# Kernel tuning notes

Hardware: AMD Instinct MI355X
Metric: run time of the kernel (lower is better)

Reference implementation:

```python
import jax, jax.numpy as jnp
import numpy as np

B, C, OUT, H, W, M1, M2, HID = 4, 64, 64, 256, 256, 32, 32, 64
COORD = C + 1  # MLP input: channels + 1 coordinate


def _lin(key, fan_in, fan_out):
    lim = 1.0 / np.sqrt(fan_in)
    kw, kb = jax.random.split(key)
    Wm = jax.random.uniform(kw, (fan_in, fan_out), minval=-lim, maxval=lim, dtype=jnp.float32)
    b = jax.random.uniform(kb, (fan_out,), minval=-lim, maxval=lim, dtype=jnp.float32)
    return Wm, b


def setup_inputs() -> dict:
    key = jax.random.key(0)
    ks = jax.random.split(key, 12)
    x = jax.random.normal(ks[0], (B, C, H, W), dtype=jnp.float32)
    # basis_w MLP: (C+1) -> HID -> HID -> 2*M2
    wW0, wb0 = _lin(ks[1], COORD, HID)
    wW1, wb1 = _lin(ks[2], HID, HID)
    wW2, wb2 = _lin(ks[3], HID, 2 * M2)
    # basis_h MLP: (C+1) -> HID -> HID -> 2*M1
    hW0, hb0 = _lin(ks[4], COORD, HID)
    hW1, hb1 = _lin(ks[5], HID, HID)
    hW2, hb2 = _lin(ks[6], HID, 2 * M1)
    std = (1.0 / (C + OUT)) ** 0.5
    Wf_re = std * jax.random.normal(ks[7], (C, OUT, M1, M2), dtype=jnp.float32)
    Wf_im = std * jax.random.normal(ks[8], (C, OUT, M1, M2), dtype=jnp.float32)
    mixer_w, mixer_b = _lin(ks[9], OUT, OUT)
    mixer_w = mixer_w.T  # (out, in) conv1x1 layout
    sc_w, sc_b = _lin(ks[10], C, OUT)
    sc_w = sc_w.T
    return {
        "x": x,
        "wW0": wW0, "wb0": wb0, "wW1": wW1, "wb1": wb1, "wW2": wW2, "wb2": wb2,
        "hW0": hW0, "hb0": hb0, "hW1": hW1, "hb1": hb1, "hW2": hW2, "hb2": hb2,
        "Wf_re": Wf_re, "Wf_im": Wf_im,
        "mixer_w": mixer_w, "mixer_b": mixer_b,
        "sc_w": sc_w, "sc_b": sc_b,
    }


def _gelu(v):
    return jax.nn.gelu(v, approximate=False)  # torch GELU is exact erf


def _cmlp(x, W0, b0, W1, b1, W2, b2, m):
    h = _gelu(x @ W0 + b0)
    h = _gelu(h @ W1 + b1)
    o = h @ W2 + b2
    return jax.lax.complex(o[..., :m], o[..., m:])


def reference(x, wW0, wb0, wW1, wb1, wW2, wb2,
              hW0, hb0, hW1, hb1, hW2, hb2,
              Wf_re, Wf_im, mixer_w, mixer_b, sc_w, sc_b):
    Bb, Cc, Hh, Ww = x.shape
    # --- W-direction basis: input is (values, w-coord) per pixel ---
    wc = jnp.linspace(-1.0, 1.0, Ww, dtype=jnp.float32)
    w_in = jnp.concatenate(
        [jnp.transpose(x, (0, 2, 3, 1)),
         jnp.broadcast_to(wc[None, None, :, None], (Bb, Hh, Ww, 1))], axis=-1)
    wb = _cmlp(w_in, wW0, wb0, wW1, wb1, wW2, wb2, M2)  # (B,H,W,m2) complex
    xc = x.astype(jnp.complex64)
    # separable transform along W: contract W against runtime basis
    tfw = jnp.einsum('bchw,bhwm->bchm', xc, wb)  # (B,C,H,m2)
    # --- H-direction basis: input is real part of W-transform + h-coord ---
    hcv = jnp.linspace(-1.0, 1.0, Hh, dtype=jnp.float32)
    h_in = jnp.concatenate(
        [jnp.transpose(tfw.real, (0, 3, 2, 1)),
         jnp.broadcast_to(hcv[None, None, :, None], (Bb, M2, Hh, 1))], axis=-1)
    hb = _cmlp(h_in, hW0, hb0, hW1, hb1, hW2, hb2, M1)  # (B,m2,H,m1) complex
    tfhw = jnp.einsum('bchm,bmhk->bckm', tfw, hb)  # (B,C,m1,m2)
    Wf = jax.lax.complex(Wf_re, Wf_im)  # (C_in, C_out, m1, m2)
    proc = jnp.einsum('bixy,oixy->boxy', tfhw, Wf)  # (B,out,m1,m2)
    # inverse transforms with conjugate-transposed bases
    rec = jnp.einsum('bokm,bmhk->bohm', proc, jnp.conj(hb))  # (B,out,H,m2)
    spatial = jnp.einsum('bohm,bhwm->bohw', rec, jnp.conj(wb)).real / (Hh * Ww)
    y = jnp.einsum('bchw,oc->bohw', spatial, mixer_w) + mixer_b[None, :, None, None]
    y = _gelu(y)
    y = y + jnp.einsum('bchw,oc->bohw', x, sc_w) + sc_b[None, :, None, None]
    return _gelu(y)
```

## Files before the change

kernel.cpp:

```cpp
#include <hip/hip_runtime.h>
#include <math.h>


typedef __attribute__((ext_vector_type(8))) short bf16x8;
typedef __attribute__((ext_vector_type(4))) float f32x4;

__device__ __forceinline__ float gelu_f(float v) {
    const float u = v * 0.70710678118654752440f;
    const float xa = fabsf(u);
    const float t = __builtin_amdgcn_rcpf(fmaf(0.3275911f, xa, 1.0f));
    float p = fmaf(1.061405429f, t, -1.453152027f);
    p = fmaf(p, t, 1.421413741f);
    p = fmaf(p, t, -0.284496736f);
    p = fmaf(p, t, 0.254829592f);
    p *= t;
    const float e = __expf(-xa * xa);
    float erfv = fmaf(-p, e, 1.0f);
    erfv = (u < 0.0f) ? -erfv : erfv;
    return 0.5f * v * (1.0f + erfv);
}

__device__ __forceinline__ unsigned short f2b(float f) {
    union { float f; unsigned int u; } v; v.f = f;
    unsigned int u = v.u + 0x7FFFu + ((v.u >> 16) & 1u);
    return (unsigned short)(u >> 16);
}
__device__ __forceinline__ float b2f(unsigned short b) {
    union { unsigned int u; float f; } v; v.u = ((unsigned int)b) << 16;
    return v.f;
}

__device__ __forceinline__ ushort4 butterfly_xT(const float4 v, int q) {
    const float bx = __shfl_xor(v.x, 1);
    const float by = __shfl_xor(v.y, 1);
    const float bz = __shfl_xor(v.z, 1);
    const float bw = __shfl_xor(v.w, 1);
    float4 s1;
    s1.x = ((q & 1) == 0) ? v.x : by;
    s1.y = ((q & 1) == 0) ? bx  : v.y;
    s1.z = ((q & 1) == 0) ? v.z : bw;
    s1.w = ((q & 1) == 0) ? bz  : v.w;
    const float cx = __shfl_xor(s1.x, 2);
    const float cy = __shfl_xor(s1.y, 2);
    const float cz = __shfl_xor(s1.z, 2);
    const float cw = __shfl_xor(s1.w, 2);
    float4 s2;
    s2.x = ((q & 2) == 0) ? s1.x : cz;
    s2.y = ((q & 2) == 0) ? s1.y : cw;
    s2.z = ((q & 2) == 0) ? cx   : s1.z;
    s2.w = ((q & 2) == 0) ? cy   : s1.w;
    ushort4 u;
    u.x = f2b(s2.x); u.y = f2b(s2.y); u.z = f2b(s2.z); u.w = f2b(s2.w);
    return u;
}

__device__ __forceinline__ void stage_xT(const float* __restrict__ x,
    unsigned short* __restrict__ sA, int b, int h, int w0, int t, int LD)
{
    const int lane = t & 63, wv = t >> 6;
    const int q = lane & 3, wg = lane >> 2;
#pragma unroll
    for (int r = 0; r < 4; ++r) {
        const int cb = (r * 4 + wv) * 4;
        const float4 v = *(const float4*)&x[((size_t)(b * 64 + cb + q) * 256 + h) * 256 + w0 + wg * 4];
        const ushort4 u = butterfly_xT(v, q);
        *(ushort4*)&sA[(wg * 4 + q) * LD + cb] = u;
    }
}

__global__ void k_prep(const float* __restrict__ wW0, const float* __restrict__ wW1,
                       const float* __restrict__ wW2,
                       const float* __restrict__ hW0, const float* __restrict__ hW1,
                       const float* __restrict__ hW2,
                       unsigned short* __restrict__ wT0, unsigned short* __restrict__ wT1,
                       unsigned short* __restrict__ wT2,
                       unsigned short* __restrict__ hT0, unsigned short* __restrict__ hT1,
                       unsigned short* __restrict__ hT2)
{
    const int t = threadIdx.x;
    for (int idx = t; idx < 64 * 96; idx += 256) {
        const int o = idx / 96, k = idx % 96;
        wT0[idx] = (k < 65) ? f2b(wW0[k * 64 + o]) : (unsigned short)0;
        hT0[idx] = (k < 65) ? f2b(hW0[k * 64 + o]) : (unsigned short)0;
    }
    for (int idx = t; idx < 4096; idx += 256) {
        const int o = idx >> 6, k = idx & 63;
        wT1[idx] = f2b(wW1[k * 64 + o]);
        wT2[idx] = f2b(wW2[k * 64 + o]);
        hT1[idx] = f2b(hW1[k * 64 + o]);
        hT2[idx] = f2b(hW2[k * 64 + o]);
    }
}

__global__ __launch_bounds__(256) void k_psum(const float* __restrict__ src,
                                              float* __restrict__ dst,
                                              int nparts, int part_stride)
{
    const int i = (blockIdx.x * 256 + threadIdx.x) * 4;
    float4 acc = *(const float4*)&src[i];
    for (int p = 1; p < nparts; ++p) {
        const float4 v = *(const float4*)&src[(size_t)p * part_stride + i];
        acc.x += v.x; acc.y += v.y; acc.z += v.z; acc.w += v.w;
    }
    *(float4*)&dst[i] = acc;
}

__global__ __launch_bounds__(256) void k_psum_procT(const float* __restrict__ src,
                                                    float* __restrict__ dst)
{
    const int idx = blockIdx.x * 256 + threadIdx.x;
    const int o = idx & 63, k = (idx >> 6) & 31, m = (idx >> 11) & 31, b = idx >> 16;
    const size_t in = (size_t)(b * 64 + o) * 1024 + k * 32 + m;
    const float re = src[in] + src[524288 + in];
    const float im = src[262144 + in] + src[524288 + 262144 + in];
    dst[idx] = re;
    dst[262144 + idx] = im;
}

template<bool GELU, int NKC>
__device__ __forceinline__ void mfma_layer_r(
    const bf16x8* __restrict__ wf,
    const unsigned short* __restrict__ sAct,
    unsigned short* __restrict__ dst,
    const float4 bv, int arow, int g, int wv)
{
    const int crow = 16 * wv + g * 4;
    const int sx7 = arow & 7, sx3 = arow & 3;
    const f32x4 zero = {0.f, 0.f, 0.f, 0.f};
    f32x4 acc[4] = {zero, zero, zero, zero};
#pragma unroll
    for (int kc = 0; kc < NKC; ++kc) {
        const int chraw = kc * 4 + g;
        const int ch = (chraw < 8) ? (chraw ^ sx7) : (8 + ((chraw - 8) ^ sx3));
#pragma unroll
        for (int nt = 0; nt < 4; ++nt) {
            const bf16x8 b = *(const bf16x8*)&sAct[(nt * 16 + arow) * 96 + ch * 8];
            acc[nt] = __builtin_amdgcn_mfma_f32_16x16x32_bf16(wf[kc], b, acc[nt], 0, 0, 0);
        }
    }
    const int chw = (crow >> 3) ^ sx7;
#pragma unroll
    for (int nt = 0; nt < 4; ++nt) {
        const int px = nt * 16 + arow;
        float v0 = acc[nt][0] + bv.x;
        float v1 = acc[nt][1] + bv.y;
        float v2 = acc[nt][2] + bv.z;
        float v3 = acc[nt][3] + bv.w;
        if (GELU) { v0 = gelu_f(v0); v1 = gelu_f(v1); v2 = gelu_f(v2); v3 = gelu_f(v3); }
        ushort4 u;
        u.x = f2b(v0); u.y = f2b(v1); u.z = f2b(v2); u.w = f2b(v3);
        *(ushort4*)&dst[px * 96 + chw * 8 + (crow & 7)] = u;
    }
}

__device__ __forceinline__ float4 load_xtile(const float* __restrict__ x,
    int b, int h, int w0, int lane, int wv, int r)
{
    const int q = lane & 3, wg = lane >> 2;
    const int cb = 16 * r + 4 * wv;
    return *(const float4*)&x[((size_t)(b * 64 + cb + q) * 256 + h) * 256 + w0 + wg * 4];
}

__global__ __launch_bounds__(256) void k_wbtfw(
    const float* __restrict__ x,
    const unsigned short* __restrict__ wT0, const float* __restrict__ b0,
    const unsigned short* __restrict__ wT1, const float* __restrict__ b1,
    const unsigned short* __restrict__ wT2, const float* __restrict__ b2,
    unsigned short* __restrict__ wb_bf, unsigned short* __restrict__ tfwM)
{
    __shared__ __align__(16) unsigned short smem[20480];
    unsigned short* sA   = smem;
    unsigned short* sB   = smem + 6144;
    unsigned short* sXt  = smem + 12288;
    unsigned short* sWBt = smem + 16384;

    const int bh = blockIdx.x;
    const int b = bh >> 8, h = bh & 255;
    const int t = threadIdx.x;
    const int lane = t & 63, wv = t >> 6;
    const int arow = lane & 15, g = lane >> 4;
    const int crow = 16 * wv + g * 4;
    const int sx7 = arow & 7;
    const f32x4 zero = {0.f, 0.f, 0.f, 0.f};

    const int wrow = 16 * wv + arow;
    bf16x8 w0f[3], w1f[2], w2f[2];
#pragma unroll
    for (int kc = 0; kc < 3; ++kc)
        w0f[kc] = *(const bf16x8*)&wT0[wrow * 96 + (kc * 4 + g) * 8];
#pragma unroll
    for (int kc = 0; kc < 2; ++kc) {
        w1f[kc] = *(const bf16x8*)&wT1[wrow * 64 + (kc * 4 + g) * 8];
        w2f[kc] = *(const bf16x8*)&wT2[wrow * 64 + (kc * 4 + g) * 8];
    }
    const float4 bv0 = *(const float4*)&b0[crow];
    const float4 bv1 = *(const float4*)&b1[crow];
    const float4 bv2 = *(const float4*)&b2[crow];

    f32x4 atf[4] = {zero, zero, zero, zero};

    float4 xv[4];
#pragma unroll
    for (int r = 0; r < 4; ++r) xv[r] = load_xtile(x, b, h, 0, lane, wv, r);

    for (int wq = 0; wq < 4; ++wq) {
        const int w0 = wq * 64;
        __syncthreads();
        {
            const int q = lane & 3, wg = lane >> 2;
#pragma unroll
            for (int r = 0; r < 4; ++r) {
                const int cb = 16 * r + 4 * wv;
                const int c = cb + q;
                const float4 v = xv[r];
                ushort4 ux;
                ux.x = f2b(v.x); ux.y = f2b(v.y); ux.z = f2b(v.z); ux.w = f2b(v.w);
                const int chx = (wg >> 1) ^ (c & 7);
                *(ushort4*)&sXt[c * 64 + chx * 8 + 4 * (wg & 1)] = ux;
                const ushort4 u = butterfly_xT(v, q);
                const int row = wg * 4 + q;
                const int cha = (cb >> 3) ^ (row & 7);
                *(ushort4*)&sA[row * 96 + cha * 8 + (cb & 7)] = u;
            }
        }
        if (t < 64) {
            const uint4 z = {0, 0, 0, 0};
#pragma unroll
            for (int j = 0; j < 4; ++j)
                *(uint4*)&sA[t * 96 + (8 + (j ^ (t & 3))) * 8] = z;
            sA[t * 96 + (8 + (t & 3)) * 8] = f2b((float)(w0 + t) * (2.0f / 255.0f) - 1.0f);
        }
        const int w0n = ((wq + 1) & 3) * 64;
        float4 xn[4];
#pragma unroll
        for (int r = 0; r < 4; ++r) xn[r] = load_xtile(x, b, h, w0n, lane, wv, r);
        __syncthreads();
        mfma_layer_r<true, 3>(w0f, sA, sB, bv0, arow, g, wv);
        __syncthreads();
        mfma_layer_r<true, 2>(w1f, sB, sA, bv1, arow, g, wv);
        __syncthreads();
        {
            f32x4 acc[4] = {zero, zero, zero, zero};
#pragma unroll
            for (int kc = 0; kc < 2; ++kc) {
                const int ch = (kc * 4 + g) ^ sx7;
#pragma unroll
                for (int nt = 0; nt < 4; ++nt) {
                    const bf16x8 bb = *(const bf16x8*)&sA[(nt * 16 + arow) * 96 + ch * 8];
                    acc[nt] = __builtin_amdgcn_mfma_f32_16x16x32_bf16(w2f[kc], bb, acc[nt], 0, 0, 0);
                }
            }
            const int chw = (crow >> 3) ^ sx7;
#pragma unroll
            for (int nt = 0; nt < 4; ++nt) {
                const int px = nt * 16 + arow;
                ushort4 u;
                u.x = f2b(acc[nt][0] + bv2.x);
                u.y = f2b(acc[nt][1] + bv2.y);
                u.z = f2b(acc[nt][2] + bv2.z);
                u.w = f2b(acc[nt][3] + bv2.w);
                *(ushort4*)&sB[px * 96 + chw * 8 + (crow & 7)] = u;
                const int ph = px >> 3, pl = px & 7;
                sWBt[(crow + 0) * 64 + ((ph ^ ((crow + 0) & 7)) << 3) + pl] = u.x;
                sWBt[(crow + 1) * 64 + ((ph ^ ((crow + 1) & 7)) << 3) + pl] = u.y;
                sWBt[(crow + 2) * 64 + ((ph ^ ((crow + 2) & 7)) << 3) + pl] = u.z;
                sWBt[(crow + 3) * 64 + ((ph ^ ((crow + 3) & 7)) << 3) + pl] = u.w;
            }
        }
        __syncthreads();
        const size_t pixbase = (size_t)(b * 256 + h) * 256 + w0;
#pragma unroll
        for (int r = 0; r < 2; ++r) {
            const int idx = r * 256 + t;
            const int px = idx >> 3, f = idx & 7;
            *(uint4*)&wb_bf[(pixbase + px) * 64 + f * 8] =
                *(const uint4*)&sB[px * 96 + ((f ^ (px & 7)) << 3)];
        }
#pragma unroll
        for (int kc = 0; kc < 2; ++kc) {
            const int ch = (kc * 4 + g) ^ sx7;
            const bf16x8 a = *(const bf16x8*)&sWBt[(16 * wv + arow) * 64 + ch * 8];
#pragma unroll
            for (int nt = 0; nt < 4; ++nt) {
                const bf16x8 bb = *(const bf16x8*)&sXt[(nt * 16 + arow) * 64 + ch * 8];
                atf[nt] = __builtin_amdgcn_mfma_f32_16x16x32_bf16(a, bb, atf[nt], 0, 0, 0);
            }
        }
#pragma unroll
        for (int r = 0; r < 4; ++r) xv[r] = xn[r];
    }

    __syncthreads();
    float* sF = (float*)smem;
#pragma unroll
    for (int nt = 0; nt < 4; ++nt) {
        const int c = nt * 16 + arow;
#pragma unroll
        for (int j = 0; j < 4; ++j)
            sF[(crow + j) * 68 + c] = atf[nt][j];
    }
    __syncthreads();
#pragma unroll
    for (int r = 0; r < 4; ++r) {
        const int idx = r * 256 + t;
        const int m = idx >> 5, gg = idx & 31;
        ushort4 u;
        u.x = f2b(sF[m * 68 + gg * 2]);
        u.y = f2b(sF[(m + 32) * 68 + gg * 2]);
        u.z = f2b(sF[m * 68 + gg * 2 + 1]);
        u.w = f2b(sF[(m + 32) * 68 + gg * 2 + 1]);
        *(ushort4*)&tfwM[((size_t)(b * 32 + m) * 256 + h) * 128 + gg * 4] = u;
    }
}

__global__ __launch_bounds__(256) void k_hb_mlp3(
    const unsigned short* __restrict__ tfwM,
    const unsigned short* __restrict__ hT0, const float* __restrict__ b0,
    const unsigned short* __restrict__ hT1, const float* __restrict__ b1,
    const unsigned short* __restrict__ hT2, const float* __restrict__ b2,
    unsigned short* __restrict__ hb_bf)
{
    __shared__ __align__(16) unsigned short sA[64 * 96];
    __shared__ __align__(16) unsigned short sB[64 * 96];
    const int blk = blockIdx.x;
    const int bm = blk >> 2, hq = blk & 3;
    const int h0 = hq * 64;
    const int t = threadIdx.x;
    const int lane = t & 63, wv = t >> 6;
    const int arow = lane & 15, g = lane >> 4;
    const int crow = 16 * wv + g * 4;

    const int wrow = 16 * wv + arow;
    bf16x8 h0f[3], h1f[2], h2f[2];
#pragma unroll
    for (int kc = 0; kc < 3; ++kc)
        h0f[kc] = *(const bf16x8*)&hT0[wrow * 96 + (kc * 4 + g) * 8];
#pragma unroll
    for (int kc = 0; kc < 2; ++kc) {
        h1f[kc] = *(const bf16x8*)&hT1[wrow * 64 + (kc * 4 + g) * 8];
        h2f[kc] = *(const bf16x8*)&hT2[wrow * 64 + (kc * 4 + g) * 8];
    }
    const float4 bv0 = *(const float4*)&b0[crow];
    const float4 bv1 = *(const float4*)&b1[crow];
    const float4 bv2 = *(const float4*)&b2[crow];

#pragma unroll
    for (int r = 0; r < 4; ++r) {
        const int idx = r * 256 + t;
        const int p = idx >> 4, f = idx & 15;
        const uint4 raw = *(const uint4*)&tfwM[((size_t)(bm * 256 + h0 + p)) * 128 + f * 8];
        const unsigned short* s = (const unsigned short*)&raw;
        ushort4 u;
        u.x = s[0]; u.y = s[2]; u.z = s[4]; u.w = s[6];
        const int ch = (f >> 1) ^ (p & 7);
        *(ushort4*)&sA[p * 96 + ch * 8 + 4 * (f & 1)] = u;
    }
    if (t < 64) {
        const uint4 z = {0, 0, 0, 0};
#pragma unroll
        for (int j = 0; j < 4; ++j)
            *(uint4*)&sA[t * 96 + (8 + (j ^ (t & 3))) * 8] = z;
        sA[t * 96 + (8 + (t & 3)) * 8] = f2b((float)(h0 + t) * (2.0f / 255.0f) - 1.0f);
    }
    __syncthreads();
    mfma_layer_r<true, 3>(h0f, sA, sB, bv0, arow, g, wv);
    __syncthreads();
    mfma_layer_r<true, 2>(h1f, sB, sA, bv1, arow, g, wv);
    __syncthreads();
    mfma_layer_r<false, 2>(h2f, sA, sB, bv2, arow, g, wv);
    __syncthreads();

    const size_t pixbase = (size_t)bm * 256 + h0;
#pragma unroll
    for (int r = 0; r < 2; ++r) {
        const int idx = r * 256 + t;
        const int px = idx >> 3, f = idx & 7;
        *(uint4*)&hb_bf[(pixbase + px) * 64 + f * 8] =
            *(const uint4*)&sB[px * 96 + ((f ^ (px & 7)) << 3)];
    }
}

__global__ __launch_bounds__(256) void k_tfhw3(
    const unsigned short* __restrict__ tfwM,
    const unsigned short* __restrict__ hb_bf,
    float* __restrict__ tfhw_p)
{
    __shared__ float hr[64 * 32];
    __shared__ float hi2[64 * 32];
    __shared__ float slab[32 * 64];
    const int blk = blockIdx.x;
    const int bm = blk >> 3, chalf = (blk >> 2) & 1, hq = blk & 3;
    const int b = bm >> 5, m = bm & 31;
    const int t = threadIdx.x;
#pragma unroll
    for (int r = 0; r < 2; ++r) {
        const int q = r * 256 + t;
        const int hl = q >> 3, f = q & 7;
        const uint4 raw = *(const uint4*)&hb_bf[((size_t)bm * 256 + hq * 64 + hl) * 64 + f * 8];
        const unsigned short* us = (const unsigned short*)&raw;
        float v[8];
#pragma unroll
        for (int j = 0; j < 8; ++j) v[j] = b2f(us[j]);
        float* dst = (f < 4) ? &hr[hl * 32 + f * 8] : &hi2[hl * 32 + (f - 4) * 8];
        float4 lo; lo.x = v[0]; lo.y = v[1]; lo.z = v[2]; lo.w = v[3];
        float4 hi; hi.x = v[4]; hi.y = v[5]; hi.z = v[6]; hi.w = v[7];
        *(float4*)&dst[0] = lo;
        *(float4*)&dst[4] = hi;
    }
    const int k = t & 31, cq = t >> 5;
    float accr[4] = {0.f, 0.f, 0.f, 0.f}, acci[4] = {0.f, 0.f, 0.f, 0.f};
    const size_t tbase = (size_t)bm * 32768;
    for (int ht = 0; ht < 2; ++ht) {
        __syncthreads();
        {
            const int hl = t >> 3, f = t & 7;
            const uint4 raw = *(const uint4*)&tfwM[tbase + (size_t)(hq * 64 + ht * 32 + hl) * 128 + chalf * 64 + f * 8];
            const unsigned short* s = (const unsigned short*)&raw;
            float4 lo, hi;
            lo.x = b2f(s[0]); lo.y = b2f(s[1]); lo.z = b2f(s[2]); lo.w = b2f(s[3]);
            hi.x = b2f(s[4]); hi.y = b2f(s[5]); hi.z = b2f(s[6]); hi.w = b2f(s[7]);
            *(float4*)&slab[hl * 64 + f * 8] = lo;
            *(float4*)&slab[hl * 64 + f * 8 + 4] = hi;
        }
        __syncthreads();
#pragma unroll 8
        for (int hl = 0; hl < 32; ++hl) {
            const float hrv = hr[(ht * 32 + hl) * 32 + k];
            const float hiv = hi2[(ht * 32 + hl) * 32 + k];
            const float4 u0 = *(const float4*)&slab[hl * 64 + cq * 8];
            const float4 u1 = *(const float4*)&slab[hl * 64 + cq * 8 + 4];
            accr[0] = fmaf(u0.x, hrv, fmaf(-u0.y, hiv, accr[0]));
            acci[0] = fmaf(u0.x, hiv, fmaf( u0.y, hrv, acci[0]));
            accr[1] = fmaf(u0.z, hrv, fmaf(-u0.w, hiv, accr[1]));
            acci[1] = fmaf(u0.z, hiv, fmaf( u0.w, hrv, acci[1]));
            accr[2] = fmaf(u1.x, hrv, fmaf(-u1.y, hiv, accr[2]));
            acci[2] = fmaf(u1.x, hiv, fmaf( u1.y, hrv, acci[2]));
            accr[3] = fmaf(u1.z, hrv, fmaf(-u1.w, hiv, accr[3]));
            acci[3] = fmaf(u1.z, hiv, fmaf( u1.w, hrv, acci[3]));
        }
    }
    float* tp = tfhw_p + (size_t)hq * 524288;
#pragma unroll
    for (int i = 0; i < 4; ++i) {
        const int c = chalf * 32 + cq * 4 + i;
        const size_t po = ((size_t)(b * 64 + c) * 32 + k) * 32 + m;
        tp[po] = accr[i];
        tp[262144 + po] = acci[i];
    }
}

__global__ __launch_bounds__(256) void k_proc2(
    const float* __restrict__ tfhw,
    const float* __restrict__ Wf_re, const float* __restrict__ Wf_im,
    float* __restrict__ proc_p)
{
    const int blk = blockIdx.x;
    const int o = blk >> 3, kq = (blk >> 1) & 3, chalf = blk & 1;
    const int t = threadIdx.x;
    const int mo = kq * 256 + t;
    const float* tre = tfhw;
    const float* tim = tfhw + 262144;
    float accr[4] = {0.f, 0.f, 0.f, 0.f}, acci[4] = {0.f, 0.f, 0.f, 0.f};
    for (int cc = 0; cc < 32; ++cc) {
        const int c = chalf * 32 + cc;
        const float wfr = Wf_re[(size_t)(c * 64 + o) * 1024 + mo];
        const float wfi = Wf_im[(size_t)(c * 64 + o) * 1024 + mo];
#pragma unroll
        for (int bb = 0; bb < 4; ++bb) {
            const float tr = tre[(size_t)(bb * 64 + c) * 1024 + mo];
            const float ti = tim[(size_t)(bb * 64 + c) * 1024 + mo];
            accr[bb] = fmaf(tr, wfr, fmaf(-ti, wfi, accr[bb]));
            acci[bb] = fmaf(tr, wfi, fmaf(ti, wfr, acci[bb]));
        }
    }
    float* pp = proc_p + (size_t)chalf * 524288;
#pragma unroll
    for (int bb = 0; bb < 4; ++bb) {
        pp[(size_t)(bb * 64 + o) * 1024 + mo] = accr[bb];
        pp[262144 + (size_t)(bb * 64 + o) * 1024 + mo] = acci[bb];
    }
}

__global__ __launch_bounds__(256) void k_rec4(
    const float* __restrict__ procT,
    const unsigned short* __restrict__ hb_bf,
    unsigned short* __restrict__ recO)
{
    __shared__ float lhr[32 * 32];
    __shared__ float lhi[32 * 32];
    const int blk = blockIdx.x;
    const int bm = blk >> 3, hq = blk & 7;
    const int b = bm >> 5, m = bm & 31;
    const int t = threadIdx.x;
    {
        const int hl = t >> 3, f = t & 7;
        const uint4 raw = *(const uint4*)&hb_bf[((size_t)bm * 256 + hq * 32 + hl) * 64 + f * 8];
        const unsigned short* us = (const unsigned short*)&raw;
        float v[8];
#pragma unroll
        for (int j = 0; j < 8; ++j) v[j] = b2f(us[j]);
        float* dst = (f < 4) ? &lhr[hl * 32 + f * 8] : &lhi[hl * 32 + (f - 4) * 8];
        float4 lo; lo.x = v[0]; lo.y = v[1]; lo.z = v[2]; lo.w = v[3];
        float4 hi; hi.x = v[4]; hi.y = v[5]; hi.z = v[6]; hi.w = v[7];
        *(float4*)&dst[0] = lo;
        *(float4*)&dst[4] = hi;
    }
    const int o = t & 63, hg = t >> 6;
    const float* pr = procT + (size_t)(b * 32 + m) * 2048 + o;
    const float* pi = pr + 262144;
    float Pr[32], Pi[32];
#pragma unroll
    for (int k = 0; k < 32; ++k) {
        Pr[k] = pr[k * 64];
        Pi[k] = pi[k * 64];
    }
    __syncthreads();
    for (int hh = 0; hh < 8; ++hh) {
        const int hl = hg * 8 + hh;
        float ar = 0.f, ai = 0.f;
#pragma unroll
        for (int k4 = 0; k4 < 8; ++k4) {
            const float4 hr4 = *(const float4*)&lhr[hl * 32 + k4 * 4];
            const float4 hi4 = *(const float4*)&lhi[hl * 32 + k4 * 4];
            ar = fmaf(Pr[k4*4+0], hr4.x, fmaf(Pi[k4*4+0], hi4.x, ar));
            ai = fmaf(Pi[k4*4+0], hr4.x, fmaf(-Pr[k4*4+0], hi4.x, ai));
            ar = fmaf(Pr[k4*4+1], hr4.y, fmaf(Pi[k4*4+1], hi4.y, ar));
            ai = fmaf(Pi[k4*4+1], hr4.y, fmaf(-Pr[k4*4+1], hi4.y, ai));
            ar = fmaf(Pr[k4*4+2], hr4.z, fmaf(Pi[k4*4+2], hi4.z, ar));
            ai = fmaf(Pi[k4*4+2], hr4.z, fmaf(-Pr[k4*4+2], hi4.z, ai));
            ar = fmaf(Pr[k4*4+3], hr4.w, fmaf(Pi[k4*4+3], hi4.w, ar));
            ai = fmaf(Pi[k4*4+3], hr4.w, fmaf(-Pr[k4*4+3], hi4.w, ai));
        }
        const int h = hq * 32 + hl;
        const size_t rb = ((size_t)(b * 256 + h) * 64 + o) * 64;
        recO[rb + m]      = f2b(ar);
        recO[rb + 32 + m] = f2b(ai);
    }
}

__global__ __launch_bounds__(256) void k_final4(
    const float* __restrict__ x,
    const unsigned short* __restrict__ wb_bf,
    const unsigned short* __restrict__ recO,
    const float* __restrict__ mw, const float* __restrict__ mb,
    const float* __restrict__ scw, const float* __restrict__ scb,
    float* __restrict__ out)
{
    constexpr int LD = 72;
    __shared__ __align__(16) unsigned short sWb[64 * LD];
    __shared__ __align__(16) unsigned short sR [64 * LD];
    __shared__ __align__(16) unsigned short sX [64 * LD];
    __shared__ __align__(16) unsigned short sS [64 * LD];
    const int blk = blockIdx.x;
    const int b = blk >> 10, h = (blk >> 2) & 255, wq = blk & 3;
    const int w0 = wq * 64;
    const int t = threadIdx.x;
    const int lane = t & 63, wv = t >> 6;
    const size_t pixbase = (size_t)(b * 256 + h) * 256 + w0;

#pragma unroll
    for (int r = 0; r < 2; ++r) {
        const int idx = r * 256 + t;
        const int px = idx >> 3, f = idx & 7;
        *(uint4*)&sWb[px * LD + f * 8] = *(const uint4*)&wb_bf[(pixbase + px) * 64 + f * 8];
    }
    const size_t recbase = (size_t)(b * 256 + h) * 4096;
#pragma unroll
    for (int r = 0; r < 2; ++r) {
        const int idx = r * 256 + t;
        const int o = idx >> 3, f = idx & 7;
        *(uint4*)&sR[o * LD + f * 8] = *(const uint4*)&recO[recbase + (size_t)o * 64 + f * 8];
    }
    stage_xT(x, sX, b, h, w0, t, LD);
    __syncthreads();

    const int arow = lane & 15;
    const int koff = (lane >> 4) * 8;
    const f32x4 zero = {0.f, 0.f, 0.f, 0.f};

    f32x4 accA[4] = {zero, zero, zero, zero};
#pragma unroll
    for (int kc = 0; kc < 2; ++kc) {
        const bf16x8 a = *(const bf16x8*)&sR[(16 * wv + arow) * LD + kc * 32 + koff];
#pragma unroll
        for (int nt = 0; nt < 4; ++nt) {
            const bf16x8 bb = *(const bf16x8*)&sWb[(nt * 16 + arow) * LD + kc * 32 + koff];
            accA[nt] = __builtin_amdgcn_mfma_f32_16x16x32_bf16(a, bb, accA[nt], 0, 0, 0);
        }
    }
    __syncthreads();

    const int crow = 16 * wv + (lane >> 4) * 4;
#pragma unroll
    for (int nt = 0; nt < 4; ++nt) {
        const int px = nt * 16 + arow;
#pragma unroll
        for (int j = 0; j < 4; ++j)
            sS[px * LD + crow + j] = f2b(accA[nt][j] * (1.0f / 65536.0f));
    }
#pragma unroll
    for (int r = 0; r < 4; ++r) {
        const int idx = r * 256 + t;
        const int o = idx >> 4, cq = idx & 15;
        const float4 v1 = *(const float4*)&mw[o * 64 + cq * 4];
        ushort4 u1;
        u1.x = f2b(v1.x); u1.y = f2b(v1.y); u1.z = f2b(v1.z); u1.w = f2b(v1.w);
        *(ushort4*)&sWb[o * LD + cq * 4] = u1;
        const float4 v2 = *(const float4*)&scw[o * 64 + cq * 4];
        ushort4 u2;
        u2.x = f2b(v2.x); u2.y = f2b(v2.y); u2.z = f2b(v2.z); u2.w = f2b(v2.w);
        *(ushort4*)&sR[o * LD + cq * 4] = u2;
    }
    __syncthreads();

    f32x4 accB[4] = {zero, zero, zero, zero};
    f32x4 accC[4] = {zero, zero, zero, zero};
#pragma unroll
    for (int kc = 0; kc < 2; ++kc) {
        const bf16x8 am = *(const bf16x8*)&sWb[(16 * wv + arow) * LD + kc * 32 + koff];
        const bf16x8 as = *(const bf16x8*)&sR [(16 * wv + arow) * LD + kc * 32 + koff];
#pragma unroll
        for (int nt = 0; nt < 4; ++nt) {
            const bf16x8 bs = *(const bf16x8*)&sS[(nt * 16 + arow) * LD + kc * 32 + koff];
            const bf16x8 bx = *(const bf16x8*)&sX[(nt * 16 + arow) * LD + kc * 32 + koff];
            accB[nt] = __builtin_amdgcn_mfma_f32_16x16x32_bf16(am, bs, accB[nt], 0, 0, 0);
            accC[nt] = __builtin_amdgcn_mfma_f32_16x16x32_bf16(as, bx, accC[nt], 0, 0, 0);
        }
    }

#pragma unroll
    for (int nt = 0; nt < 4; ++nt) {
        const int px = nt * 16 + arow;
#pragma unroll
        for (int j = 0; j < 4; ++j) {
            const int o = crow + j;
            const float y = gelu_f(accB[nt][j] + mb[o]);
            const float z = y + accC[nt][j] + scb[o];
            out[((size_t)(b * 64 + o) * 256 + h) * 256 + w0 + px] = gelu_f(z);
        }
    }
}

extern "C" void kernel_launch(void* const* d_in, const int* in_sizes, int n_in,
                              void* d_out, int out_size, void* d_ws, size_t ws_size,
                              hipStream_t stream) {
    const float* x    = (const float*)d_in[0];
    const float* wW0  = (const float*)d_in[1];
    const float* wb0  = (const float*)d_in[2];
    const float* wW1  = (const float*)d_in[3];
    const float* wb1  = (const float*)d_in[4];
    const float* wW2  = (const float*)d_in[5];
    const float* wb2  = (const float*)d_in[6];
    const float* hW0  = (const float*)d_in[7];
    const float* hb0  = (const float*)d_in[8];
    const float* hW1  = (const float*)d_in[9];
    const float* hb1  = (const float*)d_in[10];
    const float* hW2  = (const float*)d_in[11];
    const float* hb2  = (const float*)d_in[12];
    const float* Wf_re = (const float*)d_in[13];
    const float* Wf_im = (const float*)d_in[14];
    const float* mw   = (const float*)d_in[15];
    const float* mbv  = (const float*)d_in[16];
    const float* scw  = (const float*)d_in[17];
    const float* scb  = (const float*)d_in[18];

    char* base = (char*)d_ws;
    unsigned short* wb_bf = (unsigned short*)(base + 0);
    unsigned short* tfwM  = (unsigned short*)(base + 33554432);
    unsigned short* hb_bf = (unsigned short*)(base + 41943040);
    float* tfhw_p = (float*)(base + 46137344);
    float* tfhw   = (float*)(base + 54525952);
    float* proc_p = (float*)(base + 56623104);
    float* procT  = (float*)(base + 60817408);
    unsigned short* recO = (unsigned short*)(base + 62914560);
    unsigned short* wT0 = (unsigned short*)(base + 71303168);
    unsigned short* wT1 = (unsigned short*)(base + 71315456);
    unsigned short* wT2 = (unsigned short*)(base + 71323648);
    unsigned short* hT0 = (unsigned short*)(base + 71331840);
    unsigned short* hT1 = (unsigned short*)(base + 71344128);
    unsigned short* hT2 = (unsigned short*)(base + 71352320);

    k_prep<<<1, 256, 0, stream>>>(wW0, wW1, wW2, hW0, hW1, hW2,
                                  wT0, wT1, wT2, hT0, hT1, hT2);
    k_wbtfw<<<1024, 256, 0, stream>>>(x, wT0, wb0, wT1, wb1, wT2, wb2,
                                      wb_bf, tfwM);
    k_hb_mlp3<<<512, 256, 0, stream>>>(tfwM, hT0, hb0, hT1, hb1, hT2, hb2, hb_bf);
    k_tfhw3<<<1024, 256, 0, stream>>>(tfwM, hb_bf, tfhw_p);
    k_psum<<<1024, 256, 0, stream>>>(tfhw_p, tfhw, 4, 524288);
    k_proc2<<<512, 256, 0, stream>>>(tfhw, Wf_re, Wf_im, proc_p);
    k_psum_procT<<<1024, 256, 0, stream>>>(proc_p, procT);
    k_rec4<<<1024, 256, 0, stream>>>(procT, hb_bf, recO);
    k_final4<<<4096, 256, 0, stream>>>(x, wb_bf, recO, mw, mbv, scw, scb,
                                       (float*)d_out);
}
```

Baseline: 180.1 us.

## Fuse H-basis MLP with H-transform contraction and trim redundant prefetch loads

Merges the H-direction basis MLP kernel and the tfhw contraction kernel into one, so the basis computed in shared memory is consumed directly instead of being reloaded from global memory. Each fused block now covers all 64 channels per h-quarter, so it does twice the work per thread with 8 accumulators and a 512-block grid instead of 1024. It also skips the wrap-around x-tile prefetch on the last W iteration and hoists the mixer and shortcut weight loads earlier in the final kernel. The trade-off is lower parallelism and more register pressure in the contraction phase, plus bank-swizzled bf16 reads in the inner loop.

Result: no change. 177.3 us, median of 2 (-1.6%).

```diff
diff --git a/kernel.cpp b/kernel.cpp
--- a/kernel.cpp
+++ b/kernel.cpp
@@ -230,10 +230,12 @@
                 *(uint4*)&sA[t * 96 + (8 + (j ^ (t & 3))) * 8] = z;
             sA[t * 96 + (8 + (t & 3)) * 8] = f2b((float)(w0 + t) * (2.0f / 255.0f) - 1.0f);
         }
-        const int w0n = ((wq + 1) & 3) * 64;
         float4 xn[4];
-#pragma unroll
-        for (int r = 0; r < 4; ++r) xn[r] = load_xtile(x, b, h, w0n, lane, wv, r);
+        if (wq < 3) {
+            const int w0n = (wq + 1) * 64;
+#pragma unroll
+            for (int r = 0; r < 4; ++r) xn[r] = load_xtile(x, b, h, w0n, lane, wv, r);
+        }
         __syncthreads();
         mfma_layer_r<true, 3>(w0f, sA, sB, bv0, arow, g, wv);
         __syncthreads();
@@ -286,8 +288,10 @@
                 atf[nt] = __builtin_amdgcn_mfma_f32_16x16x32_bf16(a, bb, atf[nt], 0, 0, 0);
             }
         }
-#pragma unroll
-        for (int r = 0; r < 4; ++r) xv[r] = xn[r];
+        if (wq < 3) {
+#pragma unroll
+            for (int r = 0; r < 4; ++r) xv[r] = xn[r];
+        }
     }
 
     __syncthreads();
@@ -313,17 +317,21 @@
     }
 }
 
-__global__ __launch_bounds__(256) void k_hb_mlp3(
+__global__ __launch_bounds__(256) void k_hbtfhw(
     const unsigned short* __restrict__ tfwM,
     const unsigned short* __restrict__ hT0, const float* __restrict__ b0,
     const unsigned short* __restrict__ hT1, const float* __restrict__ b1,
     const unsigned short* __restrict__ hT2, const float* __restrict__ b2,
-    unsigned short* __restrict__ hb_bf)
-{
-    __shared__ __align__(16) unsigned short sA[64 * 96];
-    __shared__ __align__(16) unsigned short sB[64 * 96];
+    unsigned short* __restrict__ hb_bf, float* __restrict__ tfhw_p)
+{
+    __shared__ __align__(16) unsigned short smem[14336];
+    unsigned short* sB = smem;
+    unsigned short* sA = smem + 6144;
+    float* slab = (float*)(smem + 6144);
+
     const int blk = blockIdx.x;
     const int bm = blk >> 2, hq = blk & 3;
+    const int b = bm >> 5, m = bm & 31;
     const int h0 = hq * 64;
     const int t = threadIdx.x;
     const int lane = t & 63, wv = t >> 6;
@@ -378,71 +386,46 @@
         *(uint4*)&hb_bf[(pixbase + px) * 64 + f * 8] =
             *(const uint4*)&sB[px * 96 + ((f ^ (px & 7)) << 3)];
     }
-}
-
-__global__ __launch_bounds__(256) void k_tfhw3(
-    const unsigned short* __restrict__ tfwM,
-    const unsigned short* __restrict__ hb_bf,
-    float* __restrict__ tfhw_p)
-{
-    __shared__ float hr[64 * 32];
-    __shared__ float hi2[64 * 32];
-    __shared__ float slab[32 * 64];
-    const int blk = blockIdx.x;
-    const int bm = blk >> 3, chalf = (blk >> 2) & 1, hq = blk & 3;
-    const int b = bm >> 5, m = bm & 31;
-    const int t = threadIdx.x;
-#pragma unroll
-    for (int r = 0; r < 2; ++r) {
-        const int q = r * 256 + t;
-        const int hl = q >> 3, f = q & 7;
-        const uint4 raw = *(const uint4*)&hb_bf[((size_t)bm * 256 + hq * 64 + hl) * 64 + f * 8];
-        const unsigned short* us = (const unsigned short*)&raw;
-        float v[8];
-#pragma unroll
-        for (int j = 0; j < 8; ++j) v[j] = b2f(us[j]);
-        float* dst = (f < 4) ? &hr[hl * 32 + f * 8] : &hi2[hl * 32 + (f - 4) * 8];
-        float4 lo; lo.x = v[0]; lo.y = v[1]; lo.z = v[2]; lo.w = v[3];
-        float4 hi; hi.x = v[4]; hi.y = v[5]; hi.z = v[6]; hi.w = v[7];
-        *(float4*)&dst[0] = lo;
-        *(float4*)&dst[4] = hi;
-    }
+
     const int k = t & 31, cq = t >> 5;
-    float accr[4] = {0.f, 0.f, 0.f, 0.f}, acci[4] = {0.f, 0.f, 0.f, 0.f};
+    float accr[8], acci[8];
+#pragma unroll
+    for (int i = 0; i < 8; ++i) { accr[i] = 0.f; acci[i] = 0.f; }
     const size_t tbase = (size_t)bm * 32768;
     for (int ht = 0; ht < 2; ++ht) {
         __syncthreads();
-        {
-            const int hl = t >> 3, f = t & 7;
-            const uint4 raw = *(const uint4*)&tfwM[tbase + (size_t)(hq * 64 + ht * 32 + hl) * 128 + chalf * 64 + f * 8];
+#pragma unroll
+        for (int r = 0; r < 2; ++r) {
+            const int idx = r * 256 + t;
+            const int hl = idx >> 4, f = idx & 15;
+            const uint4 raw = *(const uint4*)&tfwM[tbase + (size_t)(h0 + ht * 32 + hl) * 128 + f * 8];
             const unsigned short* s = (const unsigned short*)&raw;
             float4 lo, hi;
             lo.x = b2f(s[0]); lo.y = b2f(s[1]); lo.z = b2f(s[2]); lo.w = b2f(s[3]);
             hi.x = b2f(s[4]); hi.y = b2f(s[5]); hi.z = b2f(s[6]); hi.w = b2f(s[7]);
-            *(float4*)&slab[hl * 64 + f * 8] = lo;
-            *(float4*)&slab[hl * 64 + f * 8 + 4] = hi;
+            *(float4*)&slab[hl * 128 + f * 8] = lo;
+            *(float4*)&slab[hl * 128 + f * 8 + 4] = hi;
         }
         __syncthreads();
 #pragma unroll 8
         for (int hl = 0; hl < 32; ++hl) {
-            const float hrv = hr[(ht * 32 + hl) * 32 + k];
-            const float hiv = hi2[(ht * 32 + hl) * 32 + k];
-            const float4 u0 = *(const float4*)&slab[hl * 64 + cq * 8];
-            const float4 u1 = *(const float4*)&slab[hl * 64 + cq * 8 + 4];
-            accr[0] = fmaf(u0.x, hrv, fmaf(-u0.y, hiv, accr[0]));
-            acci[0] = fmaf(u0.x, hiv, fmaf( u0.y, hrv, acci[0]));
-            accr[1] = fmaf(u0.z, hrv, fmaf(-u0.w, hiv, accr[1]));
-            acci[1] = fmaf(u0.z, hiv, fmaf( u0.w, hrv, acci[1]));
-            accr[2] = fmaf(u1.x, hrv, fmaf(-u1.y, hiv, accr[2]));
-            acci[2] = fmaf(u1.x, hiv, fmaf( u1.y, hrv, acci[2]));
-            accr[3] = fmaf(u1.z, hrv, fmaf(-u1.w, hiv, accr[3]));
-            acci[3] = fmaf(u1.z, hiv, fmaf( u1.w, hrv, acci[3]));
+            const int hrow = ht * 32 + hl;
+            const float hrv = b2f(sB[hrow * 96 + (((k >> 3) ^ (hrow & 7)) << 3) + (k & 7)]);
+            const float hiv = b2f(sB[hrow * 96 + ((((32 + k) >> 3) ^ (hrow & 7)) << 3) + (k & 7)]);
+#pragma unroll
+            for (int i2 = 0; i2 < 4; ++i2) {
+                const float4 u = *(const float4*)&slab[hl * 128 + cq * 16 + i2 * 4];
+                accr[i2 * 2]     = fmaf(u.x, hrv, fmaf(-u.y, hiv, accr[i2 * 2]));
+                acci[i2 * 2]     = fmaf(u.x, hiv, fmaf( u.y, hrv, acci[i2 * 2]));
+                accr[i2 * 2 + 1] = fmaf(u.z, hrv, fmaf(-u.w, hiv, accr[i2 * 2 + 1]));
+                acci[i2 * 2 + 1] = fmaf(u.z, hiv, fmaf( u.w, hrv, acci[i2 * 2 + 1]));
+            }
         }
     }
     float* tp = tfhw_p + (size_t)hq * 524288;
 #pragma unroll
-    for (int i = 0; i < 4; ++i) {
-        const int c = chalf * 32 + cq * 4 + i;
+    for (int i = 0; i < 8; ++i) {
+        const int c = cq * 8 + i;
         const size_t po = ((size_t)(b * 64 + c) * 32 + k) * 32 + m;
         tp[po] = accr[i];
         tp[262144 + po] = acci[i];
@@ -558,6 +541,15 @@
     const int lane = t & 63, wv = t >> 6;
     const size_t pixbase = (size_t)(b * 256 + h) * 256 + w0;
 
+    float4 mwv[4], scv[4];
+#pragma unroll
+    for (int r = 0; r < 4; ++r) {
+        const int idx = r * 256 + t;
+        const int o = idx >> 4, cq2 = idx & 15;
+        mwv[r] = *(const float4*)&mw[o * 64 + cq2 * 4];
+        scv[r] = *(const float4*)&scw[o * 64 + cq2 * 4];
+    }
+
 #pragma unroll
     for (int r = 0; r < 2; ++r) {
         const int idx = r * 256 + t;
@@ -601,15 +593,13 @@
 #pragma unroll
     for (int r = 0; r < 4; ++r) {
         const int idx = r * 256 + t;
-        const int o = idx >> 4, cq = idx & 15;
-        const float4 v1 = *(const float4*)&mw[o * 64 + cq * 4];
+        const int o = idx >> 4, cq2 = idx & 15;
         ushort4 u1;
-        u1.x = f2b(v1.x); u1.y = f2b(v1.y); u1.z = f2b(v1.z); u1.w = f2b(v1.w);
-        *(ushort4*)&sWb[o * LD + cq * 4] = u1;
-        const float4 v2 = *(const float4*)&scw[o * 64 + cq * 4];
+        u1.x = f2b(mwv[r].x); u1.y = f2b(mwv[r].y); u1.z = f2b(mwv[r].z); u1.w = f2b(mwv[r].w);
+        *(ushort4*)&sWb[o * LD + cq2 * 4] = u1;
         ushort4 u2;
-        u2.x = f2b(v2.x); u2.y = f2b(v2.y); u2.z = f2b(v2.z); u2.w = f2b(v2.w);
-        *(ushort4*)&sR[o * LD + cq * 4] = u2;
+        u2.x = f2b(scv[r].x); u2.y = f2b(scv[r].y); u2.z = f2b(scv[r].z); u2.w = f2b(scv[r].w);
+        *(ushort4*)&sR[o * LD + cq2 * 4] = u2;
     }
     __syncthreads();
 
@@ -684,8 +674,8 @@
                                   wT0, wT1, wT2, hT0, hT1, hT2);
     k_wbtfw<<<1024, 256, 0, stream>>>(x, wT0, wb0, wT1, wb1, wT2, wb2,
                                       wb_bf, tfwM);
-    k_hb_mlp3<<<512, 256, 0, stream>>>(tfwM, hT0, hb0, hT1, hb1, hT2, hb2, hb_bf);
-    k_tfhw3<<<1024, 256, 0, stream>>>(tfwM, hb_bf, tfhw_p);
+    k_hbtfhw<<<512, 256, 0, stream>>>(tfwM, hT0, hb0, hT1, hb1, hT2, hb2,
+                                      hb_bf, tfhw_p);
     k_psum<<<1024, 256, 0, stream>>>(tfhw_p, tfhw, 4, 524288);
     k_proc2<<<512, 256, 0, stream>>>(tfhw, Wf_re, Wf_im, proc_p);
     k_psum_procT<<<1024, 256, 0, stream>>>(proc_p, procT);
```
